# Optimization experiments

Measured on AMD Instinct MI355X. Metric: run time of the kernel, lower is better.

Reference implementation:

```python
import jax, jax.numpy as jnp
import numpy as np

N_NODES = 50000


def setup_inputs() -> dict:
    key = jax.random.key(0)
    k1, k2, k3 = jax.random.split(key, 3)
    x = jax.random.normal(k1, (N_NODES, 256), dtype=jnp.float32)
    edge_index = jax.random.randint(k2, (2, 1600000), 0, N_NODES, dtype=jnp.int64)
    W = jax.random.normal(k3, (256, 256), dtype=jnp.float32) / np.sqrt(256.0)
    b = jnp.zeros((256,), dtype=jnp.float32)
    return {"x": x, "edge_index": edge_index, "W": W, "b": b}


def reference(x, edge_index, W, b):
    # PyG GCNConv: add self-loops, symmetric normalization, linear, aggregate, bias; then ReLU.
    n = x.shape[0]
    self_loops = jnp.arange(n, dtype=edge_index.dtype)
    src = jnp.concatenate([edge_index[0], self_loops])  # [E+N]
    dst = jnp.concatenate([edge_index[1], self_loops])  # [E+N]

    # degree from incoming edges (incl. self loops)
    deg = jax.ops.segment_sum(jnp.ones_like(dst, dtype=x.dtype), dst, num_segments=n)
    dinv = jnp.where(deg > 0, jax.lax.rsqrt(deg), 0.0)
    norm = dinv[src] * dinv[dst]  # [E+N]

    xw = x @ W  # [N, out] linear first (GCNConv transforms then propagates)
    msgs = xw[src] * norm[:, None]  # gather + edge-normalize
    agg = jax.ops.segment_sum(msgs, dst, num_segments=n)  # scatter-add
    return jax.nn.relu(agg + b)
```

## Files before the change

kernel.cpp:

```cpp
#include <hip/hip_runtime.h>
#include <hip/hip_bf16.h>


#define FEATS 256
#define MAXBUCK 200
#define P1_CAP 64
#define BCAP 10240

typedef __bf16 bf16x8 __attribute__((ext_vector_type(8)));
typedef float f32x4 __attribute__((ext_vector_type(4)));

__device__ __forceinline__ unsigned short f2bf(float f) {
  unsigned u = __float_as_uint(f);
  u += 0x7fffu + ((u >> 16) & 1u);
  return (unsigned short)(u >> 16);
}
__device__ __forceinline__ float bflo(unsigned u) { return __uint_as_float(u << 16); }
__device__ __forceinline__ float bfhi(unsigned u) { return __uint_as_float(u & 0xFFFF0000u); }


__global__ __launch_bounds__(256) void zero_i32(int* __restrict__ p, int n) {
  int i = blockIdx.x * 256 + threadIdx.x;
  if (i < n) p[i] = 0;
}

__global__ __launch_bounds__(1024) void pass1_bin(const int* __restrict__ src,
                                                  const int* __restrict__ dst,
                                                  int E, int nbuck,
                                                  int* __restrict__ gcursor,
                                                  unsigned* __restrict__ temp) {
  __shared__ unsigned lbuf[MAXBUCK * P1_CAP];
  __shared__ int lcnt[MAXBUCK];
  __shared__ int lbase[MAXBUCK];
  const int tid = threadIdx.x;
  for (int i = tid; i < nbuck; i += 1024) lcnt[i] = 0;
  __syncthreads();

  const int e0 = blockIdx.x * 4096;
  #pragma unroll
  for (int i = 0; i < 4; ++i) {
    int e = e0 + i * 1024 + tid;
    if (e < E) {
      unsigned d = (unsigned)dst[e];
      unsigned p = (d << 16) | (unsigned)src[e];
      int b = (int)(d >> 8);
      int pos = atomicAdd(&lcnt[b], 1);
      if (pos < P1_CAP) {
        lbuf[b * P1_CAP + pos] = p;
      } else {
        int gp = atomicAdd(&gcursor[b], 1);
        temp[(size_t)b * BCAP + gp] = p;
      }
    }
  }
  __syncthreads();
  if (tid < nbuck) {
    int c = lcnt[tid]; if (c > P1_CAP) c = P1_CAP;
    lcnt[tid] = c;
    lbase[tid] = atomicAdd(&gcursor[tid], c);
  }
  __syncthreads();
  for (int i = tid; i < nbuck * P1_CAP; i += 1024) {
    int b = i >> 6, j = i & (P1_CAP - 1);
    if (j < lcnt[b]) temp[(size_t)b * BCAP + lbase[b] + j] = lbuf[i];
  }
}

__global__ __launch_bounds__(256) void scan_buckets(const int* __restrict__ gcursor,
                                                    int* __restrict__ bbase,
                                                    int* __restrict__ row_ptr,
                                                    int nbuck, int n) {
  __shared__ int tmp[256];
  int t = threadIdx.x;
  int v = (t < nbuck) ? min(gcursor[t], BCAP) : 0;
  tmp[t] = v;
  __syncthreads();
  #pragma unroll
  for (int off = 1; off < 256; off <<= 1) {
    int x = (t >= off) ? tmp[t - off] : 0;
    __syncthreads();
    tmp[t] += x;
    __syncthreads();
  }
  if (t < nbuck) bbase[t] = tmp[t] - v;
  if (t == 0) row_ptr[n] = tmp[255];
}

__global__ __launch_bounds__(1024) void pass2_csr(const unsigned* __restrict__ temp,
                                                  const int* __restrict__ gcursor,
                                                  const int* __restrict__ bbase,
                                                  unsigned short* __restrict__ csr16,
                                                  int* __restrict__ row_ptr,
                                                  float* __restrict__ dinv, int n) {
  __shared__ unsigned ebuf[BCAP];
  __shared__ unsigned short sorted[BCAP];
  __shared__ int hist[256], scn[256], sexcl[256], ofs[256];
  const int b = blockIdx.x;
  const int tid = threadIdx.x;
  int cnt = gcursor[b]; if (cnt > BCAP) cnt = BCAP;
  const int base = bbase[b];
  const unsigned* tp = temp + (size_t)b * BCAP;

  if (tid < 256) { hist[tid] = 0; ofs[tid] = 0; }
  for (int i = tid; i < cnt; i += 1024) ebuf[i] = tp[i];
  __syncthreads();
  for (int i = tid; i < cnt; i += 1024) atomicAdd(&hist[(ebuf[i] >> 16) & 255], 1);
  __syncthreads();

  if (tid < 256) scn[tid] = hist[tid];
  __syncthreads();
  #pragma unroll
  for (int off = 1; off < 256; off <<= 1) {
    int x = 0;
    if (tid < 256 && tid >= off) x = scn[tid - off];
    __syncthreads();
    if (tid < 256) scn[tid] += x;
    __syncthreads();
  }
  if (tid < 256) {
    int v = hist[tid];
    int excl = scn[tid] - v;
    sexcl[tid] = excl;
    int node = (b << 8) + tid;
    if (node < n) {
      row_ptr[node] = base + excl;
      dinv[node] = rsqrtf((float)(v + 1));
    }
  }
  __syncthreads();

  for (int i = tid; i < cnt; i += 1024) {
    unsigned e = ebuf[i];
    int dl = (int)((e >> 16) & 255);
    int pos = sexcl[dl] + atomicAdd(&ofs[dl], 1);
    sorted[pos] = (unsigned short)(e & 0xFFFFu);
  }
  __syncthreads();
  for (int i = tid; i < cnt; i += 1024) csr16[base + i] = sorted[i];
}


__global__ __launch_bounds__(256) void wt_build(const float* __restrict__ W,
                                                unsigned short* __restrict__ Wt) {
  int k = blockIdx.x;
  int nn = threadIdx.x;
  Wt[nn * FEATS + k] = f2bf(W[k * FEATS + nn]);
}


__global__ __launch_bounds__(256) void gemm_mfma(const float* __restrict__ x,
                                                 const unsigned short* __restrict__ Wt,
                                                 const float* __restrict__ dinv,
                                                 unsigned short* __restrict__ xwp, int M) {
  const int wave = (int)((blockIdx.x * 256 + threadIdx.x) >> 6);
  const int lane = (int)(threadIdx.x & 63);
  const int m0 = wave * 16;
  if (m0 >= M) return;
  const int lm = lane & 15;
  const int quad = lane >> 4;

  int arow = m0 + lm; if (arow >= M) arow = M - 1;
  const float* xrow = x + (size_t)arow * FEATS + quad * 8;
  bf16x8 Afrag[8];
  #pragma unroll
  for (int kc = 0; kc < 8; ++kc) {
    const float4 f0 = *(const float4*)(xrow + kc * 32);
    const float4 f1 = *(const float4*)(xrow + kc * 32 + 4);
    union { bf16x8 v; unsigned short u[8]; } a;
    a.u[0] = f2bf(f0.x); a.u[1] = f2bf(f0.y); a.u[2] = f2bf(f0.z); a.u[3] = f2bf(f0.w);
    a.u[4] = f2bf(f1.x); a.u[5] = f2bf(f1.y); a.u[6] = f2bf(f1.z); a.u[7] = f2bf(f1.w);
    Afrag[kc] = a.v;
  }

  float dsc[4];
  #pragma unroll
  for (int r = 0; r < 4; ++r) {
    int rr = m0 + quad * 4 + r; if (rr >= M) rr = M - 1;
    dsc[r] = dinv[rr];
  }

  for (int ct = 0; ct < 16; ++ct) {
    const int c0 = ct * 16;
    const unsigned short* wrow = Wt + (size_t)(c0 + lm) * FEATS + quad * 8;
    f32x4 acc = {0.f, 0.f, 0.f, 0.f};
    #pragma unroll
    for (int kc = 0; kc < 8; ++kc) {
      bf16x8 B = *(const bf16x8*)(wrow + kc * 32);
      acc = __builtin_amdgcn_mfma_f32_16x16x32_bf16(Afrag[kc], B, acc, 0, 0, 0);
    }
    #pragma unroll
    for (int r = 0; r < 4; ++r) {
      int row = m0 + quad * 4 + r;
      if (row < M) xwp[(size_t)row * FEATS + c0 + lm] = f2bf(acc[r] * dsc[r]);
    }
  }
}


__global__ __launch_bounds__(256) void aggregate(const unsigned short* __restrict__ xwp,
                                                 const float* __restrict__ dinv,
                                                 const int* __restrict__ row_ptr,
                                                 const unsigned short* __restrict__ csr16,
                                                 const float* __restrict__ bias,
                                                 float* __restrict__ out, int n) {
  const int node = (int)((blockIdx.x * blockDim.x + threadIdx.x) >> 6);
  const int lane = (int)(threadIdx.x & 63);
  if (node >= n) return;
  const int co = lane << 2;

  uint2 sv = *(const uint2*)(xwp + (((size_t)node) << 8) + co);
  float4 acc;
  acc.x = bflo(sv.x); acc.y = bfhi(sv.x); acc.z = bflo(sv.y); acc.w = bfhi(sv.y);

  const int beg = row_ptr[node];
  const int end = row_ptr[node + 1];
  for (int base = beg; base < end; base += 64) {
    int idx = base + lane;
    int s = (idx < end) ? (int)csr16[idx] : 0;
    int m = end - base;
    if (m > 64) m = 64;
    int i = 0;
    for (; i + 8 <= m; i += 8) {
      uint2 v[8];
      #pragma unroll
      for (int j = 0; j < 8; ++j) {
        int sj = __shfl(s, i + j);
        v[j] = *(const uint2*)(xwp + (((size_t)sj) << 8) + co);
      }
      #pragma unroll
      for (int j = 0; j < 8; ++j) {
        acc.x += bflo(v[j].x); acc.y += bfhi(v[j].x);
        acc.z += bflo(v[j].y); acc.w += bfhi(v[j].y);
      }
    }
    for (; i < m; ++i) {
      int sj = __shfl(s, i);
      uint2 v = *(const uint2*)(xwp + (((size_t)sj) << 8) + co);
      acc.x += bflo(v.x); acc.y += bfhi(v.x);
      acc.z += bflo(v.y); acc.w += bfhi(v.y);
    }
  }

  const float dd = dinv[node];
  const float* bp = bias + co;
  f32x4 o;
  o.x = fmaxf(fmaf(acc.x, dd, bp[0]), 0.f);
  o.y = fmaxf(fmaf(acc.y, dd, bp[1]), 0.f);
  o.z = fmaxf(fmaf(acc.z, dd, bp[2]), 0.f);
  o.w = fmaxf(fmaf(acc.w, dd, bp[3]), 0.f);
  __builtin_nontemporal_store(o, (f32x4*)(out + (((size_t)node) << 8) + co));
}


extern "C" void kernel_launch(void* const* d_in, const int* in_sizes, int n_in,
                              void* d_out, int out_size, void* d_ws, size_t ws_size,
                              hipStream_t stream) {
  const float* x  = (const float*)d_in[0];
  const int*   ei = (const int*)d_in[1];
  const float* W  = (const float*)d_in[2];
  const float* b  = (const float*)d_in[3];

  const int n = in_sizes[0] / FEATS;
  const int E = in_sizes[1] / 2;
  const int* src = ei;
  const int* dst = ei + E;
  const int nbuck = (n + 255) >> 8;

  char* ws = (char*)d_ws;
  unsigned short* xwp   = (unsigned short*)(ws);
  unsigned short* Wt    = (unsigned short*)(ws + 25600000);
  float*          dinv  = (float*)(ws + 25731072);
  int*            row_ptr = (int*)(ws + 25931072);
  unsigned short* csr16 = (unsigned short*)(ws + 26131136);
  int*            gcursor = (int*)(ws + 29331136);
  int*            bbase   = (int*)(ws + 29332160);
  unsigned*       temp    = (unsigned*)(ws + 29333184);

  hipLaunchKernelGGL(zero_i32, dim3(1), dim3(256), 0, stream, gcursor, nbuck);
  hipLaunchKernelGGL(wt_build, dim3(256), dim3(256), 0, stream, W, Wt);

  const int g_p1 = (E + 4095) / 4096;
  hipLaunchKernelGGL(pass1_bin, dim3(g_p1), dim3(1024), 0, stream, src, dst, E, nbuck, gcursor, temp);
  hipLaunchKernelGGL(scan_buckets, dim3(1), dim3(256), 0, stream, gcursor, bbase, row_ptr, nbuck, n);
  hipLaunchKernelGGL(pass2_csr, dim3(nbuck), dim3(1024), 0, stream, temp, gcursor, bbase,
                     csr16, row_ptr, dinv, n);

  const int strips = (n + 15) / 16;
  hipLaunchKernelGGL(gemm_mfma, dim3((strips + 3) / 4), dim3(256), 0, stream, x, Wt, dinv, xwp, n);

  const int g_agg = (n * 64 + 255) / 256;
  hipLaunchKernelGGL(aggregate, dim3(g_agg), dim3(256), 0, stream,
                     xwp, dinv, row_ptr, csr16, b, (float*)d_out, n);
}
```

Measured before the change: 290.6 us.

## Restructure GEMM so each wave keeps a 64-column W slice in registers and shares A via LDS

The GEMM used to have each wave own a 16-row strip and stream all 256 columns of W from global memory, so W was re-read once per strip. Now each block covers 64 rows. Each wave loads its 64-column slice of transposed W into registers once. The converted bf16 A tiles are staged in LDS and shared by all four waves, so each wave computes 4 sub-tiles with 4 independent MFMA accumulators. This cuts repeated W loads and adds MFMA-level parallelism, at the cost of heavy register pressure (a 32-entry bf16x8 B fragment array) and one block barrier.

```diff
diff --git a/kernel.cpp b/kernel.cpp
--- a/kernel.cpp
+++ b/kernel.cpp
@@ -148,50 +148,68 @@
 }
 
 
-__global__ __launch_bounds__(256) void gemm_mfma(const float* __restrict__ x,
-                                                 const unsigned short* __restrict__ Wt,
-                                                 const float* __restrict__ dinv,
-                                                 unsigned short* __restrict__ xwp, int M) {
-  const int wave = (int)((blockIdx.x * 256 + threadIdx.x) >> 6);
+__global__ __launch_bounds__(256, 2) void gemm_mfma(const float* __restrict__ x,
+                                                    const unsigned short* __restrict__ Wt,
+                                                    const float* __restrict__ dinv,
+                                                    unsigned short* __restrict__ xwp, int M) {
+  __shared__ bf16x8 A_lds[32 * 64];
+  const int wv   = (int)(threadIdx.x >> 6);
   const int lane = (int)(threadIdx.x & 63);
-  const int m0 = wave * 16;
-  if (m0 >= M) return;
-  const int lm = lane & 15;
+  const int lm   = lane & 15;
   const int quad = lane >> 4;
-
-  int arow = m0 + lm; if (arow >= M) arow = M - 1;
-  const float* xrow = x + (size_t)arow * FEATS + quad * 8;
-  bf16x8 Afrag[8];
-  #pragma unroll
-  for (int kc = 0; kc < 8; ++kc) {
-    const float4 f0 = *(const float4*)(xrow + kc * 32);
-    const float4 f1 = *(const float4*)(xrow + kc * 32 + 4);
-    union { bf16x8 v; unsigned short u[8]; } a;
-    a.u[0] = f2bf(f0.x); a.u[1] = f2bf(f0.y); a.u[2] = f2bf(f0.z); a.u[3] = f2bf(f0.w);
-    a.u[4] = f2bf(f1.x); a.u[5] = f2bf(f1.y); a.u[6] = f2bf(f1.z); a.u[7] = f2bf(f1.w);
-    Afrag[kc] = a.v;
-  }
-
-  float dsc[4];
-  #pragma unroll
-  for (int r = 0; r < 4; ++r) {
-    int rr = m0 + quad * 4 + r; if (rr >= M) rr = M - 1;
-    dsc[r] = dinv[rr];
-  }
-
-  for (int ct = 0; ct < 16; ++ct) {
-    const int c0 = ct * 16;
-    const unsigned short* wrow = Wt + (size_t)(c0 + lm) * FEATS + quad * 8;
-    f32x4 acc = {0.f, 0.f, 0.f, 0.f};
+  const int m0   = (int)blockIdx.x * 64;
+
+  bf16x8 Bfrag[4][8];
+  #pragma unroll
+  for (int ct = 0; ct < 4; ++ct) {
+    const unsigned short* wrow = Wt + (size_t)(wv * 64 + ct * 16 + lm) * FEATS + quad * 8;
+    #pragma unroll
+    for (int kc = 0; kc < 8; ++kc)
+      Bfrag[ct][kc] = *(const bf16x8*)(wrow + kc * 32);
+  }
+
+  {
+    int arow = m0 + wv * 16 + lm; if (arow >= M) arow = M - 1;
+    const float* xrow = x + (size_t)arow * FEATS + quad * 8;
     #pragma unroll
     for (int kc = 0; kc < 8; ++kc) {
-      bf16x8 B = *(const bf16x8*)(wrow + kc * 32);
-      acc = __builtin_amdgcn_mfma_f32_16x16x32_bf16(Afrag[kc], B, acc, 0, 0, 0);
-    }
+      const float4 f0 = *(const float4*)(xrow + kc * 32);
+      const float4 f1 = *(const float4*)(xrow + kc * 32 + 4);
+      union { bf16x8 v; unsigned short u[8]; } a;
+      a.u[0] = f2bf(f0.x); a.u[1] = f2bf(f0.y); a.u[2] = f2bf(f0.z); a.u[3] = f2bf(f0.w);
+      a.u[4] = f2bf(f1.x); a.u[5] = f2bf(f1.y); a.u[6] = f2bf(f1.z); a.u[7] = f2bf(f1.w);
+      A_lds[(wv * 8 + kc) * 64 + lane] = a.v;
+    }
+  }
+  __syncthreads();
+
+  #pragma unroll
+  for (int sub = 0; sub < 4; ++sub) {
+    bf16x8 Af[8];
+    #pragma unroll
+    for (int kc = 0; kc < 8; ++kc) Af[kc] = A_lds[(sub * 8 + kc) * 64 + lane];
+
+    f32x4 acc[4];
+    #pragma unroll
+    for (int ct = 0; ct < 4; ++ct) acc[ct] = (f32x4){0.f, 0.f, 0.f, 0.f};
+
+    #pragma unroll
+    for (int kc = 0; kc < 8; ++kc) {
+      #pragma unroll
+      for (int ct = 0; ct < 4; ++ct)
+        acc[ct] = __builtin_amdgcn_mfma_f32_16x16x32_bf16(Af[kc], Bfrag[ct][kc], acc[ct], 0, 0, 0);
+    }
+
     #pragma unroll
     for (int r = 0; r < 4; ++r) {
-      int row = m0 + quad * 4 + r;
-      if (row < M) xwp[(size_t)row * FEATS + c0 + lm] = f2bf(acc[r] * dsc[r]);
+      const int row = m0 + sub * 16 + quad * 4 + r;
+      if (row < M) {
+        const float dd = dinv[row];
+        unsigned short* orow = xwp + (size_t)row * FEATS + wv * 64 + lm;
+        #pragma unroll
+        for (int ct = 0; ct < 4; ++ct)
+          orow[ct * 16] = f2bf(acc[ct][r] * dd);
+      }
     }
   }
 }
@@ -285,8 +303,7 @@
   hipLaunchKernelGGL(pass2_csr, dim3(nbuck), dim3(1024), 0, stream, temp, gcursor, bbase,
                      csr16, row_ptr, dinv, n);
 
-  const int strips = (n + 15) / 16;
-  hipLaunchKernelGGL(gemm_mfma, dim3((strips + 3) / 4), dim3(256), 0, stream, x, Wt, dinv, xwp, n);
+  hipLaunchKernelGGL(gemm_mfma, dim3((n + 63) / 64), dim3(256), 0, stream, x, Wt, dinv, xwp, n);
 
   const int g_agg = (n * 64 + 255) / 256;
   hipLaunchKernelGGL(aggregate, dim3(g_agg), dim3(256), 0, stream,
```

Result: faster. 256.2 us (-11.9%).
